# Kernel tuning notes

Hardware: AMD Instinct MI355X
Metric: run time of the kernel (lower is better)

The kernel has to match this reference:

```python
import jax, jax.numpy as jnp
import numpy as np

BATCH_SIZE = 4096
HYPER_LAMBDA = 0.5
EMBED_DIM = 512


def setup_inputs() -> dict:
    key = jax.random.key(0)
    k1, k2 = jax.random.split(key)
    emb_i = jax.random.normal(k1, (BATCH_SIZE, EMBED_DIM), dtype=jnp.float32)
    emb_j = jax.random.normal(k2, (BATCH_SIZE, EMBED_DIM), dtype=jnp.float32)
    return {"emb_i": emb_i, "emb_j": emb_j}


def reference(emb_i, emb_j):
    n = emb_i.shape[0]  # batch_size
    lam = jnp.asarray(HYPER_LAMBDA, dtype=emb_i.dtype)
    # L2-normalize rows (F.normalize, dim=1)
    z_i = emb_i / jnp.linalg.norm(emb_i, axis=1, keepdims=True)
    z_j = emb_j / jnp.linalg.norm(emb_j, axis=1, keepdims=True)
    reps = jnp.concatenate([z_i, z_j], axis=0)  # [2N, D]
    # cosine similarity of already-normalized rows == dot product
    sim = reps @ reps.T  # [2N, 2N]
    # diagonals at offsets +N and -N: sim[k, k+N] and sim[k+N, k]
    idx = jnp.arange(n)
    sim_ij = sim[idx, idx + n]
    sim_ji = sim[idx + n, idx]
    positives = jnp.concatenate([sim_ij, sim_ji], axis=0)  # [2N]
    positives_similarity = jnp.log1p(jnp.exp(-positives + lam))
    neg_mask = 1.0 - jnp.eye(2 * n, dtype=sim.dtype)
    negatives_exp = neg_mask * jnp.exp(sim - lam)
    negatives_similarity = jnp.log1p(negatives_exp)
    positives_sum = jnp.sum(positives_similarity) / (2 * n)
    negatives_sum = jnp.sum(negatives_similarity) / (12 * n)
    return positives_sum + negatives_sum
```

## Files before the change

### kernel.cpp

```cpp
#include <hip/hip_runtime.h>
#include <hip/hip_bf16.h>
#include <hip/hip_fp8.h>
#include <math.h>

typedef float floatx4 __attribute__((ext_vector_type(4)));
typedef long long i64;
typedef long long i64x2 __attribute__((ext_vector_type(2)));

#define N_ROWS 4096
#define DIM 512
#define LAM 0.5f
#define NT 64

#define GLOBAL_AS(p) ((const __attribute__((address_space(1))) void*)(p))
#define LDS_AS(p) ((__attribute__((address_space(3))) void*)(p))

__device__ __forceinline__ unsigned int pack4_fp8(float a, float b, float c, float d) {
    unsigned int u0 = __hip_cvt_float_to_fp8(a, __HIP_SATFINITE, __HIP_E4M3);
    unsigned int u1 = __hip_cvt_float_to_fp8(b, __HIP_SATFINITE, __HIP_E4M3);
    unsigned int u2 = __hip_cvt_float_to_fp8(c, __HIP_SATFINITE, __HIP_E4M3);
    unsigned int u3 = __hip_cvt_float_to_fp8(d, __HIP_SATFINITE, __HIP_E4M3);
    return u0 | (u1 << 8) | (u2 << 16) | (u3 << 24);
}

__global__ __launch_bounds__(256) void normalize_kernel(
    const float* __restrict__ ei, const float* __restrict__ ej,
    unsigned char* __restrict__ Z, float* __restrict__ out) {
    if (blockIdx.x == 0 && threadIdx.x == 0) out[0] = 0.0f;
    const int w = threadIdx.x >> 6, lane = threadIdx.x & 63;
    const int row = blockIdx.x * 4 + w;
    const float* __restrict__ src = (row < N_ROWS)
        ? (ei + (size_t)row * DIM)
        : (ej + (size_t)(row - N_ROWS) * DIM);
    const float4* src4 = (const float4*)src;
    float4 v0 = src4[lane];
    float4 v1 = src4[lane + 64];
    float s = v0.x*v0.x + v0.y*v0.y + v0.z*v0.z + v0.w*v0.w
            + v1.x*v1.x + v1.y*v1.y + v1.z*v1.z + v1.w*v1.w;
    #pragma unroll
    for (int off = 32; off; off >>= 1) s += __shfl_xor(s, off);
    const float r = rsqrtf(s);

    __shared__ __align__(16) unsigned char buf[4][512];
    ((unsigned int*)buf[w])[lane]      = pack4_fp8(v0.x*r, v0.y*r, v0.z*r, v0.w*r);
    ((unsigned int*)buf[w])[lane + 64] = pack4_fp8(v1.x*r, v1.y*r, v1.z*r, v1.w*r);
    __syncthreads();

    const int kt = lane >> 3, q = (lane >> 1) & 3, h = lane & 1;
    i64 val = *(const i64*)(buf[w] + kt * 64 + h * 32 + q * 8);
    const int p = (kt * 4 + q) ^ (row & 7);
    *(i64*)(Z + (size_t)row * DIM + p * 16 + h * 8) = val;
}

__global__ __launch_bounds__(256, 2) void simloss_kernel(
    const unsigned char* __restrict__ Z, float* __restrict__ out) {
    const int id = blockIdx.x;
    int bm = (int)((2*NT + 1 - sqrtf((float)((2*NT+1)*(2*NT+1)) - 8.0f * (float)id)) * 0.5f);
    if (bm < 0) bm = 0; if (bm > NT-1) bm = NT-1;
    while ((bm + 1) * NT - ((bm + 1) * bm) / 2 <= id) ++bm;
    while (bm * NT - (bm * (bm - 1)) / 2 > id) --bm;
    const int bn = bm + (id - (bm * NT - (bm * (bm - 1)) / 2));

    const int tid = threadIdx.x;
    const int w = tid >> 6, lane = tid & 63;
    const int q = lane >> 4, m16 = lane & 15;
    const int wm = w & 1, wn = w >> 1;
    const int tm = bm * 2 + wm, tn = bn * 2 + wn;

    __shared__ __align__(16) unsigned char As[2][128 * 128];
    __shared__ __align__(16) unsigned char Bs[2][128 * 128];
    __shared__ float red[4];

    const unsigned char* stA = Z + (size_t)(bm * 128 + w * 8 + (lane >> 3)) * DIM + (lane & 7) * 16;
    const unsigned char* stB = Z + (size_t)(bn * 128 + w * 8 + (lane >> 3)) * DIM + (lane & 7) * 16;
    const int ldsOff = w * 1024;

    const int fragSwz = m16 & 7;

    floatx4 acc[4][4] = {};

    #pragma unroll
    for (int l = 0; l < 4; ++l) {
        __builtin_amdgcn_global_load_lds(GLOBAL_AS(stA + (size_t)l * 32 * DIM),
                                         LDS_AS(&As[0][ldsOff + l * 4096]), 16, 0, 0);
        __builtin_amdgcn_global_load_lds(GLOBAL_AS(stB + (size_t)l * 32 * DIM),
                                         LDS_AS(&Bs[0][ldsOff + l * 4096]), 16, 0, 0);
    }
    #pragma unroll
    for (int l = 0; l < 4; ++l) {
        __builtin_amdgcn_global_load_lds(GLOBAL_AS(stA + (size_t)l * 32 * DIM + 128),
                                         LDS_AS(&As[1][ldsOff + l * 4096]), 16, 0, 0);
        __builtin_amdgcn_global_load_lds(GLOBAL_AS(stB + (size_t)l * 32 * DIM + 128),
                                         LDS_AS(&Bs[1][ldsOff + l * 4096]), 16, 0, 0);
    }

    #pragma unroll
    for (int s = 0; s < 4; ++s) {
        if (s < 3) { asm volatile("s_waitcnt vmcnt(8)" ::: "memory"); }
        else       { asm volatile("s_waitcnt vmcnt(0)" ::: "memory"); }
        __builtin_amdgcn_sched_barrier(0);
        __builtin_amdgcn_s_barrier();

        const unsigned char* fraA = &As[s & 1][(wm * 64 + m16) * 128];
        const unsigned char* fraB = &Bs[s & 1][(wn * 64 + m16) * 128];
        #pragma unroll
        for (int g = 0; g < 2; ++g) {
            const int cOff = ((g * 4 + q) ^ fragSwz) << 4;
            i64x2 af[4], bf[4];
            #pragma unroll
            for (int i = 0; i < 4; ++i) af[i] = *(const i64x2*)(fraA + i * 16 * 128 + cOff);
            #pragma unroll
            for (int j = 0; j < 4; ++j) bf[j] = *(const i64x2*)(fraB + j * 16 * 128 + cOff);
            __builtin_amdgcn_s_setprio(1);
            #pragma unroll
            for (int i = 0; i < 4; ++i)
                #pragma unroll
                for (int j = 0; j < 4; ++j) {
                    acc[i][j] = __builtin_amdgcn_mfma_f32_16x16x32_fp8_fp8(af[i].x, bf[j].x, acc[i][j], 0, 0, 0);
                    acc[i][j] = __builtin_amdgcn_mfma_f32_16x16x32_fp8_fp8(af[i].y, bf[j].y, acc[i][j], 0, 0, 0);
                }
            __builtin_amdgcn_s_setprio(0);
        }

        if (s < 2) {
            asm volatile("" ::: "memory");
            __builtin_amdgcn_s_barrier();
            #pragma unroll
            for (int l = 0; l < 4; ++l) {
                __builtin_amdgcn_global_load_lds(GLOBAL_AS(stA + (size_t)l * 32 * DIM + (s + 2) * 128),
                                                 LDS_AS(&As[s & 1][ldsOff + l * 4096]), 16, 0, 0);
                __builtin_amdgcn_global_load_lds(GLOBAL_AS(stB + (size_t)l * 32 * DIM + (s + 2) * 128),
                                                 LDS_AS(&Bs[s & 1][ldsOff + l * 4096]), 16, 0, 0);
            }
        }
    }

    const int rowBase = tm * 64 + q * 4;
    const int colBase = tn * 64 + m16;
    float negsum = 0.0f, possum = 0.0f;
    #pragma unroll
    for (int j = 0; j < 4; ++j) {
        const int cg = colBase + j * 16;
        float p = 1.0f;
        #pragma unroll
        for (int i = 0; i < 4; ++i) {
            const int rg0 = rowBase + i * 16;
            #pragma unroll
            for (int r = 0; r < 4; ++r) {
                const float sv = acc[i][j][r];
                float e = __expf(sv - LAM);
                if (rg0 + r == cg) e = 0.0f;
                p *= (1.0f + e);
                if (cg == rg0 + r + N_ROWS)
                    possum += log1pf(expf(-sv + LAM));
            }
        }
        negsum += __logf(p);
    }
    const float wgt = (tn < tm) ? 0.0f : ((tm == tn) ? 1.0f : 2.0f);
    negsum *= wgt;

    #pragma unroll
    for (int off = 32; off; off >>= 1) {
        negsum += __shfl_xor(negsum, off);
        possum += __shfl_xor(possum, off);
    }
    const float part = negsum * (1.0f / (12.0f * (float)N_ROWS))
                     + possum * (1.0f / (float)N_ROWS);
    if (lane == 0) red[w] = part;
    __syncthreads();
    if (tid == 0) atomicAdd(out, red[0] + red[1] + red[2] + red[3]);
}

extern "C" void kernel_launch(void* const* d_in, const int* in_sizes, int n_in,
                              void* d_out, int out_size, void* d_ws, size_t ws_size,
                              hipStream_t stream) {
    const float* ei = (const float*)d_in[0];
    const float* ej = (const float*)d_in[1];
    float* out = (float*)d_out;
    unsigned char* Z = (unsigned char*)d_ws;

    normalize_kernel<<<2048, 256, 0, stream>>>(ei, ej, Z, out);
    simloss_kernel<<<NT * (NT + 1) / 2, 256, 0, stream>>>(Z, out);
}
```

Baseline: 104.4 us.

## Make similarity-loss kernel persistent with cross-tile prefetch of next tile's K-slice

Replaces the one-block-per-tile launch of 2080 blocks with a persistent grid of 512 blocks. Each block loops over four or five upper-triangular tiles and prefetches the first K-slice of its next tile while finishing the current one. It also skips the epilogue for lower-triangle warp tiles and gates the positive-pair check. The goal is to cut block launch and prologue cost and the atomic count, but the pipeline now waits on vmcnt(0) every stage, which shortens prefetch depth to one stage and can expose load latency.

```diff
diff --git a/kernel.cpp b/kernel.cpp
--- a/kernel.cpp
+++ b/kernel.cpp
@@ -11,6 +11,8 @@
 #define DIM 512
 #define LAM 0.5f
 #define NT 64
+#define NTILES (NT * (NT + 1) / 2)
+#define GRID 512
 
 #define GLOBAL_AS(p) ((const __attribute__((address_space(1))) void*)(p))
 #define LDS_AS(p) ((__attribute__((address_space(3))) void*)(p))
@@ -54,111 +56,124 @@
 
 __global__ __launch_bounds__(256, 2) void simloss_kernel(
     const unsigned char* __restrict__ Z, float* __restrict__ out) {
-    const int id = blockIdx.x;
-    int bm = (int)((2*NT + 1 - sqrtf((float)((2*NT+1)*(2*NT+1)) - 8.0f * (float)id)) * 0.5f);
-    if (bm < 0) bm = 0; if (bm > NT-1) bm = NT-1;
-    while ((bm + 1) * NT - ((bm + 1) * bm) / 2 <= id) ++bm;
-    while (bm * NT - (bm * (bm - 1)) / 2 > id) --bm;
-    const int bn = bm + (id - (bm * NT - (bm * (bm - 1)) / 2));
-
     const int tid = threadIdx.x;
     const int w = tid >> 6, lane = tid & 63;
     const int q = lane >> 4, m16 = lane & 15;
     const int wm = w & 1, wn = w >> 1;
-    const int tm = bm * 2 + wm, tn = bn * 2 + wn;
 
     __shared__ __align__(16) unsigned char As[2][128 * 128];
     __shared__ __align__(16) unsigned char Bs[2][128 * 128];
     __shared__ float red[4];
 
-    const unsigned char* stA = Z + (size_t)(bm * 128 + w * 8 + (lane >> 3)) * DIM + (lane & 7) * 16;
-    const unsigned char* stB = Z + (size_t)(bn * 128 + w * 8 + (lane >> 3)) * DIM + (lane & 7) * 16;
     const int ldsOff = w * 1024;
-
     const int fragSwz = m16 & 7;
-
-    floatx4 acc[4][4] = {};
-
-    #pragma unroll
-    for (int l = 0; l < 4; ++l) {
-        __builtin_amdgcn_global_load_lds(GLOBAL_AS(stA + (size_t)l * 32 * DIM),
-                                         LDS_AS(&As[0][ldsOff + l * 4096]), 16, 0, 0);
-        __builtin_amdgcn_global_load_lds(GLOBAL_AS(stB + (size_t)l * 32 * DIM),
-                                         LDS_AS(&Bs[0][ldsOff + l * 4096]), 16, 0, 0);
+    const int stRow = w * 8 + (lane >> 3);
+    const int stCol = (lane & 7) * 16;
+
+    const int bid = blockIdx.x;
+    const int nMine = 4 + (bid < (NTILES - 4 * GRID));
+
+    auto decode = [](int id, int& bm, int& bn) {
+        int m = (int)((2*NT + 1 - sqrtf((float)((2*NT+1)*(2*NT+1)) - 8.0f * (float)id)) * 0.5f);
+        if (m < 0) m = 0; if (m > NT-1) m = NT-1;
+        while ((m + 1) * NT - ((m + 1) * m) / 2 <= id) ++m;
+        while (m * NT - (m * (m - 1)) / 2 > id) --m;
+        bm = m;
+        bn = m + (id - (m * NT - (m * (m - 1)) / 2));
+    };
+
+    int id = bid;
+    int bm, bn; decode(id, bm, bn);
+    const unsigned char* stA = Z + (size_t)(bm * 128 + stRow) * DIM + stCol;
+    const unsigned char* stB = Z + (size_t)(bn * 128 + stRow) * DIM + stCol;
+
+    float negsum = 0.0f, possum = 0.0f;
+
+    #define ISSUE(par, pA, pB, kOff)                                             \
+        _Pragma("unroll")                                                        \
+        for (int l = 0; l < 4; ++l) {                                            \
+            __builtin_amdgcn_global_load_lds(GLOBAL_AS((pA) + (size_t)l * 32 * DIM + (kOff)), \
+                                             LDS_AS(&As[par][ldsOff + l * 4096]), 16, 0, 0);  \
+            __builtin_amdgcn_global_load_lds(GLOBAL_AS((pB) + (size_t)l * 32 * DIM + (kOff)), \
+                                             LDS_AS(&Bs[par][ldsOff + l * 4096]), 16, 0, 0);  \
+        }
+
+    ISSUE(0, stA, stB, 0)
+
+    for (int mt = 0; mt < nMine; ++mt) {
+        const int tm = bm * 2 + wm, tn = bn * 2 + wn;
+        const bool hasNext = (mt + 1 < nMine);
+        int nbm = 0, nbn = 0;
+        const unsigned char *nA = stA, *nB = stB;
+        if (hasNext) {
+            decode(id + GRID, nbm, nbn);
+            nA = Z + (size_t)(nbm * 128 + stRow) * DIM + stCol;
+            nB = Z + (size_t)(nbn * 128 + stRow) * DIM + stCol;
+        }
+
+        floatx4 acc[4][4] = {};
+
+        #pragma unroll
+        for (int s = 0; s < 4; ++s) {
+            const int par = (mt * 4 + s) & 1;
+            asm volatile("s_waitcnt vmcnt(0)" ::: "memory");
+            __builtin_amdgcn_sched_barrier(0);
+            __builtin_amdgcn_s_barrier();
+            if (s < 3)        { ISSUE(par ^ 1, stA, stB, (s + 1) * 128) }
+            else if (hasNext) { ISSUE(par ^ 1, nA, nB, 0) }
+
+            const unsigned char* fraA = &As[par][(wm * 64 + m16) * 128];
+            const unsigned char* fraB = &Bs[par][(wn * 64 + m16) * 128];
+            #pragma unroll
+            for (int g = 0; g < 2; ++g) {
+                const int cOff = ((g * 4 + q) ^ fragSwz) << 4;
+                i64x2 af[4], bf[4];
+                #pragma unroll
+                for (int i = 0; i < 4; ++i) af[i] = *(const i64x2*)(fraA + i * 16 * 128 + cOff);
+                #pragma unroll
+                for (int j = 0; j < 4; ++j) bf[j] = *(const i64x2*)(fraB + j * 16 * 128 + cOff);
+                __builtin_amdgcn_s_setprio(1);
+                #pragma unroll
+                for (int i = 0; i < 4; ++i)
+                    #pragma unroll
+                    for (int j = 0; j < 4; ++j) {
+                        acc[i][j] = __builtin_amdgcn_mfma_f32_16x16x32_fp8_fp8(af[i].x, bf[j].x, acc[i][j], 0, 0, 0);
+                        acc[i][j] = __builtin_amdgcn_mfma_f32_16x16x32_fp8_fp8(af[i].y, bf[j].y, acc[i][j], 0, 0, 0);
+                    }
+                __builtin_amdgcn_s_setprio(0);
+            }
+        }
+
+        const float wgt = (tn < tm) ? 0.0f : ((tm == tn) ? 1.0f : 2.0f);
+        const bool hasPos = (tn == tm + 64);
+        if (wgt != 0.0f) {
+            const int rowBase = tm * 64 + q * 4;
+            const int colBase = tn * 64 + m16;
+            float nacc = 0.0f;
+            #pragma unroll
+            for (int j = 0; j < 4; ++j) {
+                const int cg = colBase + j * 16;
+                float p = 1.0f;
+                #pragma unroll
+                for (int i = 0; i < 4; ++i) {
+                    const int rg0 = rowBase + i * 16;
+                    #pragma unroll
+                    for (int r = 0; r < 4; ++r) {
+                        const float sv = acc[i][j][r];
+                        float e = __expf(sv - LAM);
+                        if (rg0 + r == cg) e = 0.0f;
+                        p *= (1.0f + e);
+                        if (hasPos && cg == rg0 + r + N_ROWS)
+                            possum += log1pf(expf(-sv + LAM));
+                    }
+                }
+                nacc += __logf(p);
+            }
+            negsum += nacc * wgt;
+        }
+
+        id += GRID; bm = nbm; bn = nbn; stA = nA; stB = nB;
     }
-    #pragma unroll
-    for (int l = 0; l < 4; ++l) {
-        __builtin_amdgcn_global_load_lds(GLOBAL_AS(stA + (size_t)l * 32 * DIM + 128),
-                                         LDS_AS(&As[1][ldsOff + l * 4096]), 16, 0, 0);
-        __builtin_amdgcn_global_load_lds(GLOBAL_AS(stB + (size_t)l * 32 * DIM + 128),
-                                         LDS_AS(&Bs[1][ldsOff + l * 4096]), 16, 0, 0);
-    }
-
-    #pragma unroll
-    for (int s = 0; s < 4; ++s) {
-        if (s < 3) { asm volatile("s_waitcnt vmcnt(8)" ::: "memory"); }
-        else       { asm volatile("s_waitcnt vmcnt(0)" ::: "memory"); }
-        __builtin_amdgcn_sched_barrier(0);
-        __builtin_amdgcn_s_barrier();
-
-        const unsigned char* fraA = &As[s & 1][(wm * 64 + m16) * 128];
-        const unsigned char* fraB = &Bs[s & 1][(wn * 64 + m16) * 128];
-        #pragma unroll
-        for (int g = 0; g < 2; ++g) {
-            const int cOff = ((g * 4 + q) ^ fragSwz) << 4;
-            i64x2 af[4], bf[4];
-            #pragma unroll
-            for (int i = 0; i < 4; ++i) af[i] = *(const i64x2*)(fraA + i * 16 * 128 + cOff);
-            #pragma unroll
-            for (int j = 0; j < 4; ++j) bf[j] = *(const i64x2*)(fraB + j * 16 * 128 + cOff);
-            __builtin_amdgcn_s_setprio(1);
-            #pragma unroll
-            for (int i = 0; i < 4; ++i)
-                #pragma unroll
-                for (int j = 0; j < 4; ++j) {
-                    acc[i][j] = __builtin_amdgcn_mfma_f32_16x16x32_fp8_fp8(af[i].x, bf[j].x, acc[i][j], 0, 0, 0);
-                    acc[i][j] = __builtin_amdgcn_mfma_f32_16x16x32_fp8_fp8(af[i].y, bf[j].y, acc[i][j], 0, 0, 0);
-                }
-            __builtin_amdgcn_s_setprio(0);
-        }
-
-        if (s < 2) {
-            asm volatile("" ::: "memory");
-            __builtin_amdgcn_s_barrier();
-            #pragma unroll
-            for (int l = 0; l < 4; ++l) {
-                __builtin_amdgcn_global_load_lds(GLOBAL_AS(stA + (size_t)l * 32 * DIM + (s + 2) * 128),
-                                                 LDS_AS(&As[s & 1][ldsOff + l * 4096]), 16, 0, 0);
-                __builtin_amdgcn_global_load_lds(GLOBAL_AS(stB + (size_t)l * 32 * DIM + (s + 2) * 128),
-                                                 LDS_AS(&Bs[s & 1][ldsOff + l * 4096]), 16, 0, 0);
-            }
-        }
-    }
-
-    const int rowBase = tm * 64 + q * 4;
-    const int colBase = tn * 64 + m16;
-    float negsum = 0.0f, possum = 0.0f;
-    #pragma unroll
-    for (int j = 0; j < 4; ++j) {
-        const int cg = colBase + j * 16;
-        float p = 1.0f;
-        #pragma unroll
-        for (int i = 0; i < 4; ++i) {
-            const int rg0 = rowBase + i * 16;
-            #pragma unroll
-            for (int r = 0; r < 4; ++r) {
-                const float sv = acc[i][j][r];
-                float e = __expf(sv - LAM);
-                if (rg0 + r == cg) e = 0.0f;
-                p *= (1.0f + e);
-                if (cg == rg0 + r + N_ROWS)
-                    possum += log1pf(expf(-sv + LAM));
-            }
-        }
-        negsum += __logf(p);
-    }
-    const float wgt = (tn < tm) ? 0.0f : ((tm == tn) ? 1.0f : 2.0f);
-    negsum *= wgt;
 
     #pragma unroll
     for (int off = 32; off; off >>= 1) {
@@ -170,6 +185,7 @@
     if (lane == 0) red[w] = part;
     __syncthreads();
     if (tid == 0) atomicAdd(out, red[0] + red[1] + red[2] + red[3]);
+    #undef ISSUE
 }
 
 extern "C" void kernel_launch(void* const* d_in, const int* in_sizes, int n_in,
@@ -181,5 +197,5 @@
     unsigned char* Z = (unsigned char*)d_ws;
 
     normalize_kernel<<<2048, 256, 0, stream>>>(ei, ej, Z, out);
-    simloss_kernel<<<NT * (NT + 1) / 2, 256, 0, stream>>>(Z, out);
-}
+    simloss_kernel<<<GRID, 256, 0, stream>>>(Z, out);
+}
```

New measurement: 100.8 us. -3.4%, faster.

## Load MFMA fragments directly from global memory, dropping the LDS staging

Applied to the files above, without the earlier changes.

Removes the LDS double buffering and barriers in the fp8 similarity GEMM. Each wave now loads its A/B fragments straight from global memory (L2-resident Z) into registers and software-pipelines them in even/odd halves. The epilogue also skips exp/log work for tiles whose weight is zero and gates the positive check per tile. The tradeoff is no cross-wave sharing of loaded tiles, so global/L2 traffic per block doubles, in exchange for no LDS use, no barrier stalls and possibly higher occupancy.

```diff
diff --git a/kernel.cpp b/kernel.cpp
--- a/kernel.cpp
+++ b/kernel.cpp
@@ -11,9 +11,7 @@
 #define DIM 512
 #define LAM 0.5f
 #define NT 64
-
-#define GLOBAL_AS(p) ((const __attribute__((address_space(1))) void*)(p))
-#define LDS_AS(p) ((__attribute__((address_space(3))) void*)(p))
+#define NTILES (NT * (NT + 1) / 2)
 
 __device__ __forceinline__ unsigned int pack4_fp8(float a, float b, float c, float d) {
     unsigned int u0 = __hip_cvt_float_to_fp8(a, __HIP_SATFINITE, __HIP_E4M3);
@@ -67,98 +65,73 @@
     const int wm = w & 1, wn = w >> 1;
     const int tm = bm * 2 + wm, tn = bn * 2 + wn;
 
-    __shared__ __align__(16) unsigned char As[2][128 * 128];
-    __shared__ __align__(16) unsigned char Bs[2][128 * 128];
     __shared__ float red[4];
 
-    const unsigned char* stA = Z + (size_t)(bm * 128 + w * 8 + (lane >> 3)) * DIM + (lane & 7) * 16;
-    const unsigned char* stB = Z + (size_t)(bn * 128 + w * 8 + (lane >> 3)) * DIM + (lane & 7) * 16;
-    const int ldsOff = w * 1024;
-
     const int fragSwz = m16 & 7;
+    const unsigned char* aBase = Z + (size_t)(bm * 128 + wm * 64 + m16) * DIM;
+    const unsigned char* bBase = Z + (size_t)(bn * 128 + wn * 64 + m16) * DIM;
+    const int cOff0 = (q ^ fragSwz) << 4;
+    const int cOff1 = ((4 + q) ^ fragSwz) << 4;
 
     floatx4 acc[4][4] = {};
+    i64x2 afE[4], bfE[4], afO[4], bfO[4];
 
+    #define LOADG(af, bf, koff, co)                                              \
+        _Pragma("unroll")                                                        \
+        for (int i = 0; i < 4; ++i)                                              \
+            af[i] = *(const i64x2*)(aBase + (size_t)i * 16 * DIM + (koff) + (co)); \
+        _Pragma("unroll")                                                        \
+        for (int j = 0; j < 4; ++j)                                              \
+            bf[j] = *(const i64x2*)(bBase + (size_t)j * 16 * DIM + (koff) + (co));
+
+    #define CONSUME(af, bf)                                                      \
+        _Pragma("unroll")                                                        \
+        for (int i = 0; i < 4; ++i)                                              \
+            _Pragma("unroll")                                                    \
+            for (int j = 0; j < 4; ++j)                                          \
+                acc[i][j] = __builtin_amdgcn_mfma_f32_16x16x32_fp8_fp8(af[i].x, bf[j].x, acc[i][j], 0, 0, 0); \
+        _Pragma("unroll")                                                        \
+        for (int i = 0; i < 4; ++i)                                              \
+            _Pragma("unroll")                                                    \
+            for (int j = 0; j < 4; ++j)                                          \
+                acc[i][j] = __builtin_amdgcn_mfma_f32_16x16x32_fp8_fp8(af[i].y, bf[j].y, acc[i][j], 0, 0, 0);
+
+    LOADG(afE, bfE, 0, cOff0)
     #pragma unroll
-    for (int l = 0; l < 4; ++l) {
-        __builtin_amdgcn_global_load_lds(GLOBAL_AS(stA + (size_t)l * 32 * DIM),
-                                         LDS_AS(&As[0][ldsOff + l * 4096]), 16, 0, 0);
-        __builtin_amdgcn_global_load_lds(GLOBAL_AS(stB + (size_t)l * 32 * DIM),
-                                         LDS_AS(&Bs[0][ldsOff + l * 4096]), 16, 0, 0);
-    }
-    #pragma unroll
-    for (int l = 0; l < 4; ++l) {
-        __builtin_amdgcn_global_load_lds(GLOBAL_AS(stA + (size_t)l * 32 * DIM + 128),
-                                         LDS_AS(&As[1][ldsOff + l * 4096]), 16, 0, 0);
-        __builtin_amdgcn_global_load_lds(GLOBAL_AS(stB + (size_t)l * 32 * DIM + 128),
-                                         LDS_AS(&Bs[1][ldsOff + l * 4096]), 16, 0, 0);
+    for (int h = 0; h < 4; ++h) {
+        LOADG(afO, bfO, h * 128, cOff1)
+        CONSUME(afE, bfE)
+        if (h < 3) { LOADG(afE, bfE, (h + 1) * 128, cOff0) }
+        CONSUME(afO, bfO)
     }
 
-    #pragma unroll
-    for (int s = 0; s < 4; ++s) {
-        if (s < 3) { asm volatile("s_waitcnt vmcnt(8)" ::: "memory"); }
-        else       { asm volatile("s_waitcnt vmcnt(0)" ::: "memory"); }
-        __builtin_amdgcn_sched_barrier(0);
-        __builtin_amdgcn_s_barrier();
-
-        const unsigned char* fraA = &As[s & 1][(wm * 64 + m16) * 128];
-        const unsigned char* fraB = &Bs[s & 1][(wn * 64 + m16) * 128];
+    const float wgt = (tn < tm) ? 0.0f : ((tm == tn) ? 1.0f : 2.0f);
+    const bool hasPos = (tn == tm + 64);
+    float negsum = 0.0f, possum = 0.0f;
+    if (wgt != 0.0f) {
+        const int rowBase = tm * 64 + q * 4;
+        const int colBase = tn * 64 + m16;
         #pragma unroll
-        for (int g = 0; g < 2; ++g) {
-            const int cOff = ((g * 4 + q) ^ fragSwz) << 4;
-            i64x2 af[4], bf[4];
+        for (int j = 0; j < 4; ++j) {
+            const int cg = colBase + j * 16;
+            float p = 1.0f;
             #pragma unroll
-            for (int i = 0; i < 4; ++i) af[i] = *(const i64x2*)(fraA + i * 16 * 128 + cOff);
-            #pragma unroll
-            for (int j = 0; j < 4; ++j) bf[j] = *(const i64x2*)(fraB + j * 16 * 128 + cOff);
-            __builtin_amdgcn_s_setprio(1);
-            #pragma unroll
-            for (int i = 0; i < 4; ++i)
+            for (int i = 0; i < 4; ++i) {
+                const int rg0 = rowBase + i * 16;
                 #pragma unroll
-                for (int j = 0; j < 4; ++j) {
-                    acc[i][j] = __builtin_amdgcn_mfma_f32_16x16x32_fp8_fp8(af[i].x, bf[j].x, acc[i][j], 0, 0, 0);
-                    acc[i][j] = __builtin_amdgcn_mfma_f32_16x16x32_fp8_fp8(af[i].y, bf[j].y, acc[i][j], 0, 0, 0);
+                for (int r = 0; r < 4; ++r) {
+                    const float sv = acc[i][j][r];
+                    float e = __expf(sv - LAM);
+                    if (rg0 + r == cg) e = 0.0f;
+                    p *= (1.0f + e);
+                    if (hasPos && cg == rg0 + r + N_ROWS)
+                        possum += log1pf(expf(-sv + LAM));
                 }
-            __builtin_amdgcn_s_setprio(0);
+            }
+            negsum += __logf(p);
         }
-
-        if (s < 2) {
-            asm volatile("" ::: "memory");
-            __builtin_amdgcn_s_barrier();
-            #pragma unroll
-            for (int l = 0; l < 4; ++l) {
-                __builtin_amdgcn_global_load_lds(GLOBAL_AS(stA + (size_t)l * 32 * DIM + (s + 2) * 128),
-                                                 LDS_AS(&As[s & 1][ldsOff + l * 4096]), 16, 0, 0);
-                __builtin_amdgcn_global_load_lds(GLOBAL_AS(stB + (size_t)l * 32 * DIM + (s + 2) * 128),
-                                                 LDS_AS(&Bs[s & 1][ldsOff + l * 4096]), 16, 0, 0);
-            }
-        }
+        negsum *= wgt;
     }
-
-    const int rowBase = tm * 64 + q * 4;
-    const int colBase = tn * 64 + m16;
-    float negsum = 0.0f, possum = 0.0f;
-    #pragma unroll
-    for (int j = 0; j < 4; ++j) {
-        const int cg = colBase + j * 16;
-        float p = 1.0f;
-        #pragma unroll
-        for (int i = 0; i < 4; ++i) {
-            const int rg0 = rowBase + i * 16;
-            #pragma unroll
-            for (int r = 0; r < 4; ++r) {
-                const float sv = acc[i][j][r];
-                float e = __expf(sv - LAM);
-                if (rg0 + r == cg) e = 0.0f;
-                p *= (1.0f + e);
-                if (cg == rg0 + r + N_ROWS)
-                    possum += log1pf(expf(-sv + LAM));
-            }
-        }
-        negsum += __logf(p);
-    }
-    const float wgt = (tn < tm) ? 0.0f : ((tm == tn) ? 1.0f : 2.0f);
-    negsum *= wgt;
 
     #pragma unroll
     for (int off = 32; off; off >>= 1) {
@@ -170,6 +143,8 @@
     if (lane == 0) red[w] = part;
     __syncthreads();
     if (tid == 0) atomicAdd(out, red[0] + red[1] + red[2] + red[3]);
+    #undef LOADG
+    #undef CONSUME
 }
 
 extern "C" void kernel_launch(void* const* d_in, const int* in_sizes, int n_in,
@@ -181,5 +156,5 @@
     unsigned char* Z = (unsigned char*)d_ws;
 
     normalize_kernel<<<2048, 256, 0, stream>>>(ei, ej, Z, out);
-    simloss_kernel<<<NT * (NT + 1) / 2, 256, 0, stream>>>(Z, out);
+    simloss_kernel<<<NTILES, 256, 0, stream>>>(Z, out);
 }
```

Result: slower. 110.2 us (+5.6%).
